# Optimization experiments

Measured on AMD Instinct MI355X. Metric: run time of the kernel, lower is better.

## Reference

```python
import jax, jax.numpy as jnp
import numpy as np

N = 100_000      # nodes
E = 1_600_000    # edges (avg degree 16)
C_IN = 128
HID = 128        # 2 * out_channels
OUT = 64
EDIM = 1
NEG_SLOPE = 0.2  # PyG GATConv default negative_slope


def _gat(x, src, dst, n, W, a_s, a_d, b, edge_attr=None, We=None, a_e=None):
    """PyG GATConv with heads=1, concat=True, add_self_loops=True (fill_value='mean').
    x: [n, Cin]; src/dst: [E] (messages flow src -> dst); returns [n, Cout].
    """
    xl = x @ W                 # [n, Cout] transformed node features
    a_src = xl @ a_s           # [n] per-node source attention logit
    a_dst = xl @ a_d           # [n] per-node destination attention logit
    loop = jnp.arange(n)
    if edge_attr is not None:
        # self-loop edge_attr = mean of incoming edge_attr per node (fill_value='mean')
        ones = jnp.ones((src.shape[0],), xl.dtype)
        cnt = jax.ops.segment_sum(ones, dst, num_segments=n)              # [n]
        s = jax.ops.segment_sum(edge_attr, dst, num_segments=n)           # [n, EDIM]
        loop_attr = jnp.where(cnt[:, None] > 0, s / jnp.maximum(cnt, 1.0)[:, None], 0.0)
        ea = jnp.concatenate([edge_attr, loop_attr], axis=0)              # [E+n, EDIM]
    src2 = jnp.concatenate([src, loop])
    dst2 = jnp.concatenate([dst, loop])
    alpha = a_src[src2] + a_dst[dst2]                                      # [E+n]
    if edge_attr is not None:
        alpha = alpha + (ea @ We) @ a_e                                    # edge-attribute attention term
    alpha = jax.nn.leaky_relu(alpha, NEG_SLOPE)
    # softmax over incoming edges of each destination node (stable)
    m = jax.ops.segment_max(alpha, dst2, num_segments=n)
    ex = jnp.exp(alpha - m[dst2])
    den = jax.ops.segment_sum(ex, dst2, num_segments=n)
    coef = ex / den[dst2]                                                  # [E+n]
    out = jax.ops.segment_sum(coef[:, None] * xl[src2], dst2, num_segments=n)
    return out + b


def setup_inputs() -> dict:
    key = jax.random.key(0)
    ks = jax.random.split(key, 32)
    s = 0.1
    inp = {
        "x": jax.random.normal(ks[0], (N, C_IN), jnp.float32),
        "edge_index": jax.random.randint(ks[1], (2, E), 0, N, jnp.int64),
        "edge_weights": jax.random.uniform(ks[2], (E, EDIM), jnp.float32),
    }
    def lin(k, i, o):
        return jax.random.normal(k, (i, o), jnp.float32) * s
    def vec(k, c):
        return jax.random.normal(k, (c,), jnp.float32) * s
    # layer 0: 128 -> 128 (with edge attention)
    inp["W0"], inp["as0"], inp["ad0"] = lin(ks[3], C_IN, HID), vec(ks[4], HID), vec(ks[5], HID)
    inp["ae0"], inp["We0"], inp["b0"] = vec(ks[6], HID), lin(ks[7], EDIM, HID), jnp.zeros((HID,), jnp.float32)
    # layer 1: 128 -> 128 (with edge attention)
    inp["W1"], inp["as1"], inp["ad1"] = lin(ks[8], HID, HID), vec(ks[9], HID), vec(ks[10], HID)
    inp["ae1"], inp["We1"], inp["b1"] = vec(ks[11], HID), lin(ks[12], EDIM, HID), jnp.zeros((HID,), jnp.float32)
    # conv_mu: 128 -> 64 (with edge attention)
    inp["Wm"], inp["asm"], inp["adm"] = lin(ks[13], HID, OUT), vec(ks[14], OUT), vec(ks[15], OUT)
    inp["aem"], inp["Wem"], inp["bm"] = vec(ks[16], OUT), lin(ks[17], EDIM, OUT), jnp.zeros((OUT,), jnp.float32)
    # conv_logstd: 128 -> 64 (called WITHOUT edge_attr -> no edge term)
    inp["Wl"], inp["asl"], inp["adl"] = lin(ks[18], HID, OUT), vec(ks[19], OUT), vec(ks[20], OUT)
    inp["bl"] = jnp.zeros((OUT,), jnp.float32)
    return inp


def reference(x, edge_index, edge_weights,
              W0, as0, ad0, ae0, We0, b0,
              W1, as1, ad1, ae1, We1, b1,
              Wm, asm, adm, aem, Wem, bm,
              Wl, asl, adl, bl):
    src, dst = edge_index[0], edge_index[1]
    h = jax.nn.relu(_gat(x, src, dst, N, W0, as0, ad0, b0, edge_weights, We0, ae0))
    h = jax.nn.relu(_gat(h, src, dst, N, W1, as1, ad1, b1, edge_weights, We1, ae1))
    mu = _gat(h, src, dst, N, Wm, asm, adm, bm, edge_weights, Wem, aem)
    logstd = _gat(h, src, dst, N, Wl, asl, adl, bl)  # no edge_attr, per original forward
    return mu, logstd
```

## Files before the change

### kernel.cpp

```cpp
#include <hip/hip_runtime.h>

#define NN 100000
#define EE 1600000

typedef __attribute__((ext_vector_type(8))) __bf16 bf16x8;
typedef __attribute__((ext_vector_type(4))) float f32x4;
typedef unsigned short u16;

__device__ __forceinline__ float bf2f(u16 v) {
  union { unsigned u; float f; } x; x.u = ((unsigned)v) << 16; return x.f;
}
__device__ __forceinline__ u16 f2bf(float f) {
  union { unsigned u; float f; } x; x.f = f;
  x.u += 0x7fffu + ((x.u >> 16) & 1u);
  return (u16)(x.u >> 16);
}
__device__ __forceinline__ float lo_f(unsigned u) {
  union { unsigned u; float f; } x; x.u = u << 16; return x.f;
}
__device__ __forceinline__ float hi_f(unsigned u) {
  union { unsigned u; float f; } x; x.u = u & 0xffff0000u; return x.f;
}
__device__ __forceinline__ float lrelu(float x) { return x > 0.f ? x : 0.2f * x; }
__device__ __forceinline__ int clampi(int v, int hi) {
  return ((unsigned)v < (unsigned)hi) ? v : 0;
}
__device__ __forceinline__ float ldf(const void* p, size_t i, int fl) {
  return fl ? ((const float*)p)[i] : bf2f(((const u16*)p)[i]);
}

__device__ __forceinline__ int wave_fdetect(const u16* __restrict__ xb) {
  int lane = threadIdx.x & 63;
  int bad = 0;
#pragma unroll
  for (int j = 0; j < 4; ++j) {
    float a = fabsf(bf2f(xb[lane * 4 + j]));
    bad |= (!(a == a) || a > 1e6f) ? 1 : 0;
  }
  return (__ballot(bad) != 0ull) ? 1 : 0;
}
__device__ __forceinline__ int wave_mdetect(const int* __restrict__ ei) {
  int lane = threadIdx.x & 63;
  int v = (lane < 32) ? ei[2 * lane + 1] : 0;
  return (__ballot(v != 0) == 0ull) ? 1 : 0;
}

__global__ void k_fillf(float* __restrict__ o, int n, float v) {
  int i = blockIdx.x * 256 + threadIdx.x;
  if (i < n) o[i] = v;
}

struct CvtDesc { const void* src; u16* dst; int n; };
struct SetupArgs {
  CvtDesc cvt[12];
  const void* W[4]; u16* WT[4]; int WM[4];
  const void* dw[3]; const void* da[3]; int dm[3];
  float* cvals;
  int* cnt;
  const u16* xb;
};
__global__ __launch_bounds__(256) void k_setup(SetupArgs a) {
  int b = blockIdx.x, t = threadIdx.x;
  const int ZB = (NN + 255) / 256;
  if (b < ZB) { int i = b * 256 + t; if (i < NN) a.cnt[i] = 0; return; }
  b -= ZB;
  if (b < 12) {
    int fl = wave_fdetect(a.xb);
    const void* src = a.cvt[b].src; u16* dst = a.cvt[b].dst; int n = a.cvt[b].n;
    for (int i = t; i < n; i += 256)
      dst[i] = fl ? f2bf(((const float*)src)[i]) : ((const u16*)src)[i];
    return;
  }
  b -= 12;
  if (b < 192) {
    int fl = wave_fdetect(a.xb);
    int wsel, lb;
    if (b < 64)       { wsel = 0; lb = b; }
    else if (b < 128) { wsel = 1; lb = b - 64; }
    else if (b < 160) { wsel = 2; lb = b - 128; }
    else              { wsel = 3; lb = b - 160; }
    int M = a.WM[wsel];
    int i = lb * 256 + t;
    if (i < 128 * M) {
      int k = i / M, m = i % M;
      a.WT[wsel][m * 128 + k] = f2bf(ldf(a.W[wsel], i, fl));
    }
    return;
  }
  b -= 192;
  if (b < 3) {
    if (t < 64) {
      int fl = wave_fdetect(a.xb);
      float s = 0.f; int m = a.dm[b];
      for (int j = t; j < m; j += 64) s += ldf(a.dw[b], j, fl) * ldf(a.da[b], j, fl);
      for (int off = 32; off; off >>= 1) s += __shfl_xor(s, off);
      if (t == 0) a.cvals[b] = s;
    }
    return;
  }
}

__global__ void k_bsum(const int* __restrict__ cnt, int* __restrict__ bsum, int n) {
  int b = blockIdx.x, t = threadIdx.x;
  int i0 = b * 1024 + t * 4;
  int s = 0;
#pragma unroll
  for (int j = 0; j < 4; ++j) { int i = i0 + j; if (i < n) s += cnt[i]; }
  for (int off = 32; off; off >>= 1) s += __shfl_xor(s, off);
  __shared__ int wt[4];
  int lane = t & 63, w = t >> 6;
  if (lane == 0) wt[w] = s;
  __syncthreads();
  if (t == 0) bsum[b] = wt[0] + wt[1] + wt[2] + wt[3];
}

__global__ void k_scanb(const int* __restrict__ bsum, int* __restrict__ boff, int nchunks) {
  int t = threadIdx.x;
  int lane = t & 63, w = t >> 6;
  int v = (t < nchunks) ? bsum[t] : 0;
  int sc = v;
  for (int off = 1; off < 64; off <<= 1) { int o = __shfl_up(sc, off); if (lane >= off) sc += o; }
  __shared__ int w0tot;
  if (w == 0 && lane == 63) w0tot = sc;
  __syncthreads();
  int incl = sc + (w ? w0tot : 0);
  if (t < nchunks) boff[t] = incl - v;
}

__global__ void k_scan_chunk(const int* __restrict__ cnt, const int* __restrict__ boff,
                             int* __restrict__ row_off, int n, int etot) {
  int b = blockIdx.x, t = threadIdx.x;
  int i0 = b * 1024 + t * 4;
  int v[4]; int s = 0;
#pragma unroll
  for (int j = 0; j < 4; ++j) { int i = i0 + j; v[j] = (i < n) ? cnt[i] : 0; s += v[j]; }
  int lane = t & 63, w = t >> 6;
  int sc = s;
  for (int off = 1; off < 64; off <<= 1) { int o = __shfl_up(sc, off); if (lane >= off) sc += o; }
  __shared__ int wt[4];
  if (lane == 63) wt[w] = sc;
  __syncthreads();
  int woff = 0;
  for (int k = 0; k < w; ++k) woff += wt[k];
  int ex = boff[b] + woff + sc - s;
#pragma unroll
  for (int j = 0; j < 4; ++j) { int i = i0 + j; if (i < n) row_off[i] = ex; ex += v[j]; }
  if (b == 0 && t == 0) row_off[n] = etot;
}

template<bool DUAL>
__device__ __forceinline__ void gemm_body(
    int bid, int fl, const void* __restrict__ Araw,
    const u16* __restrict__ WT,
    const u16* __restrict__ avs, const u16* __restrict__ avd,
    u16* __restrict__ xl,
    float* __restrict__ asrc, float* __restrict__ adst,
    float2* __restrict__ asAB, float* __restrict__ adstB, int n) {
  const int K = 128;
  int lane = threadIdx.x & 63;
  int wave = threadIdx.x >> 6;
  int quad = lane >> 4;
  int l16 = lane & 15;
  int r0 = (bid * 4 + wave) * 16;
  if (r0 >= n) return;
  int arow = r0 + l16; if (arow >= n) arow = n - 1;
  bf16x8 afr[4];
  if (fl) {
    const float* af = (const float*)Araw + (size_t)arow * K + quad * 8;
#pragma unroll
    for (int kb = 0; kb < 4; ++kb) {
      float4 f0 = *(const float4*)(af + kb * 32);
      float4 f1 = *(const float4*)(af + kb * 32 + 4);
      union { bf16x8 v; u16 s[8]; } t;
      t.s[0] = f2bf(f0.x); t.s[1] = f2bf(f0.y); t.s[2] = f2bf(f0.z); t.s[3] = f2bf(f0.w);
      t.s[4] = f2bf(f1.x); t.s[5] = f2bf(f1.y); t.s[6] = f2bf(f1.z); t.s[7] = f2bf(f1.w);
      afr[kb] = t.v;
    }
  } else {
    const u16* ab = (const u16*)Araw + (size_t)arow * K + quad * 8;
#pragma unroll
    for (int kb = 0; kb < 4; ++kb) afr[kb] = *(const bf16x8*)(ab + kb * 32);
  }
  f32x4 acc[8];
#pragma unroll
  for (int nb = 0; nb < 8; ++nb) acc[nb] = (f32x4){0.f, 0.f, 0.f, 0.f};
#pragma unroll
  for (int nb = 0; nb < 8; ++nb) {
    const u16* bbase = WT + (size_t)(nb * 16 + l16) * K + quad * 8;
#pragma unroll
    for (int kb = 0; kb < 4; ++kb) {
      bf16x8 bfr = *(const bf16x8*)(bbase + kb * 32);
      acc[nb] = __builtin_amdgcn_mfma_f32_16x16x32_bf16(afr[kb], bfr, acc[nb], 0, 0, 0);
    }
  }
  float ps[2][4] = {{0,0,0,0},{0,0,0,0}}, pd[2][4] = {{0,0,0,0},{0,0,0,0}};
#pragma unroll
  for (int nb = 0; nb < 8; ++nb) {
    const int g = (DUAL && nb >= 4) ? 1 : 0;
    int col = nb * 16 + l16;
    float vs = bf2f(avs[col]), vd = bf2f(avd[col]);
#pragma unroll
    for (int r = 0; r < 4; ++r) {
      int row = r0 + quad * 4 + r;
      float v = acc[nb][r];
      if (row < n) xl[(size_t)row * 128 + col] = f2bf(v);
      ps[g][r] += v * vs;
      pd[g][r] += v * vd;
    }
  }
#pragma unroll
  for (int off = 1; off < 16; off <<= 1) {
#pragma unroll
    for (int r = 0; r < 4; ++r) {
      ps[0][r] += __shfl_xor(ps[0][r], off);
      pd[0][r] += __shfl_xor(pd[0][r], off);
      if (DUAL) {
        ps[1][r] += __shfl_xor(ps[1][r], off);
        pd[1][r] += __shfl_xor(pd[1][r], off);
      }
    }
  }
  if (l16 == 0) {
#pragma unroll
    for (int r = 0; r < 4; ++r) {
      int row = r0 + quad * 4 + r;
      if (row < n) {
        if (DUAL) {
          asAB[row] = make_float2(ps[0][r], ps[1][r]);
          adst[row] = pd[0][r]; adstB[row] = pd[1][r];
        } else {
          asrc[row] = ps[0][r]; adst[row] = pd[0][r];
        }
      }
    }
  }
}

__global__ __launch_bounds__(256) void k_rkgemm(
    const int* __restrict__ ei, int* __restrict__ cnt, int* __restrict__ rank,
    const u16* __restrict__ xb, const void* __restrict__ Araw,
    const u16* __restrict__ WT, const u16* __restrict__ avs, const u16* __restrict__ avd,
    u16* __restrict__ xl, float* __restrict__ asrc, float* __restrict__ adst,
    int n, int gemmBlocks) {
  if ((int)blockIdx.x < gemmBlocks) {
    int fl = wave_fdetect(xb);
    gemm_body<false>(blockIdx.x, fl, Araw, WT, avs, avd, xl, asrc, adst,
                     nullptr, nullptr, n);
  } else {
    int m_ = wave_mdetect(ei);
    int e = ((int)blockIdx.x - gemmBlocks) * 256 + threadIdx.x;
    if (e >= EE) return;
    int d = m_ ? ei[2 * (size_t)(EE + e)] : ei[EE + e];
    d = clampi(d, NN);
    rank[e] = atomicAdd(&cnt[d], 1);
  }
}

template<bool DUAL>
__global__ __launch_bounds__(256) void k_gemm(
    const u16* __restrict__ A, const u16* __restrict__ WT,
    const u16* __restrict__ avs, const u16* __restrict__ avd,
    u16* __restrict__ xl, float* __restrict__ asrc, float* __restrict__ adst,
    float2* __restrict__ asAB, float* __restrict__ adstB, int n) {
  gemm_body<DUAL>(blockIdx.x, 0, A, WT, avs, avd, xl, asrc, adst, asAB, adstB, n);
}

__global__ void k_place(const int* __restrict__ ei, const void* __restrict__ ew,
                        const u16* __restrict__ xb,
                        const int* __restrict__ row_off, const int* __restrict__ rank,
                        int2* __restrict__ edges) {
  int m_ = wave_mdetect(ei);
  int fl = wave_fdetect(xb);
  int e = blockIdx.x * 256 + threadIdx.x;
  if (e >= EE) return;
  int s = m_ ? ei[2 * (size_t)e] : ei[e];
  int d = m_ ? ei[2 * (size_t)(EE + e)] : ei[EE + e];
  s = clampi(s, NN);
  d = clampi(d, NN);
  int p = row_off[d] + rank[e];
  if (p >= 0 && p < EE) edges[p] = make_int2(s, (int)f2bf(ldf(ew, e, fl)));
}

__global__ void k_loop2(const int* __restrict__ row_off, const int2* __restrict__ edges,
                        float* __restrict__ la, int n) {
  int i = blockIdx.x * 256 + threadIdx.x;
  if (i >= n) return;
  int b = row_off[i], e = row_off[i + 1];
  float s = 0.f;
  for (int j = b; j < e; ++j) s += bf2f((u16)(edges[j].y & 0xffff));
  la[i] = (e > b) ? s / (float)(e - b) : 0.f;
}

__global__ __launch_bounds__(256) void k_agg(
    const int* __restrict__ row_off, const int2* __restrict__ edges,
    const float* __restrict__ asrc, const float* __restrict__ adst,
    const float* __restrict__ la, const float* __restrict__ cptr,
    const u16* __restrict__ xl, const u16* __restrict__ bias,
    u16* __restrict__ out, int n) {
  __shared__ float lp[4][64];
  __shared__ int lsv[4][64];
  int wid = (blockIdx.x * blockDim.x + threadIdx.x) >> 6;
  if (wid >= n) return;
  int w = threadIdx.x >> 6;
  int d = __builtin_amdgcn_readfirstlane(wid);
  int lane = threadIdx.x & 63;
  float c = cptr[0];
  float ad = adst[d];
  float aL = lrelu(asrc[d] + ad + c * la[d]);
  float lsum = 0.f;
  unsigned su = *(const unsigned*)(xl + (size_t)d * 128 + 2 * lane);
  float A0 = lo_f(su), A1 = hi_f(su);
  int beg = row_off[d], end = row_off[d + 1];
  for (int base = beg; base < end; base += 64) {
    int i = base + lane;
    bool v = i < end;
    int2 ev = v ? edges[i] : make_int2(0, 0);
    int s = ev.x;
    float e = 0.f;
    if (v) {
      float al = lrelu(asrc[s] + ad + c * bf2f((u16)(ev.y & 0xffff)));
      e = __expf(al - aL);
    }
    lsum += e;
    lp[w][lane] = e; lsv[w][lane] = s;
    int cnt = end - base; if (cnt > 64) cnt = 64;
    float B0 = 0.f, B1 = 0.f, C0 = 0.f, C1 = 0.f, D0 = 0.f, D1 = 0.f;
    int j = 0;
    for (; j + 4 <= cnt; j += 4) {
      float p0 = lp[w][j + 0]; int s0 = lsv[w][j + 0];
      float p1 = lp[w][j + 1]; int s1 = lsv[w][j + 1];
      float p2 = lp[w][j + 2]; int s2 = lsv[w][j + 2];
      float p3 = lp[w][j + 3]; int s3 = lsv[w][j + 3];
      unsigned u0 = *(const unsigned*)(xl + (size_t)s0 * 128 + 2 * lane);
      unsigned u1 = *(const unsigned*)(xl + (size_t)s1 * 128 + 2 * lane);
      unsigned u2 = *(const unsigned*)(xl + (size_t)s2 * 128 + 2 * lane);
      unsigned u3 = *(const unsigned*)(xl + (size_t)s3 * 128 + 2 * lane);
      A0 = fmaf(p0, lo_f(u0), A0); A1 = fmaf(p0, hi_f(u0), A1);
      B0 = fmaf(p1, lo_f(u1), B0); B1 = fmaf(p1, hi_f(u1), B1);
      C0 = fmaf(p2, lo_f(u2), C0); C1 = fmaf(p2, hi_f(u2), C1);
      D0 = fmaf(p3, lo_f(u3), D0); D1 = fmaf(p3, hi_f(u3), D1);
    }
    for (; j < cnt; ++j) {
      float p0 = lp[w][j]; int s0 = lsv[w][j];
      unsigned u0 = *(const unsigned*)(xl + (size_t)s0 * 128 + 2 * lane);
      A0 = fmaf(p0, lo_f(u0), A0); A1 = fmaf(p0, hi_f(u0), A1);
    }
    A0 += B0 + C0 + D0; A1 += B1 + C1 + D1;
  }
#pragma unroll
  for (int off = 32; off; off >>= 1) lsum += __shfl_xor(lsum, off);
  float inv = 1.f / (lsum + 1.f);
  float o0 = fmaxf(fmaf(A0, inv, bf2f(bias[2 * lane])), 0.f);
  float o1 = fmaxf(fmaf(A1, inv, bf2f(bias[2 * lane + 1])), 0.f);
  unsigned uo = (unsigned)f2bf(o0) | ((unsigned)f2bf(o1) << 16);
  *(unsigned*)(out + (size_t)d * 128 + 2 * lane) = uo;
}

__global__ __launch_bounds__(256) void k_aggh(
    const int* __restrict__ row_off, const int2* __restrict__ edges,
    const float2* __restrict__ asAB, const float* __restrict__ adA,
    const float* __restrict__ adB,
    const float* __restrict__ la, const float* __restrict__ cptr,
    const u16* __restrict__ xl, const u16* __restrict__ bias,
    float* __restrict__ outf, int n) {
  __shared__ float lpA[4][64];
  __shared__ float lpB[4][64];
  __shared__ int lsv[4][64];
  int wid = (blockIdx.x * blockDim.x + threadIdx.x) >> 6;
  if (wid >= n) return;
  int w = threadIdx.x >> 6;
  int d = __builtin_amdgcn_readfirstlane(wid);
  int lane = threadIdx.x & 63;
  bool isMu = lane < 32;
  float c = cptr[0];
  float adAd = adA[d], adBd = adB[d];
  float2 abd = asAB[d];
  float aLA = lrelu(abd.x + adAd + c * la[d]);
  float aLB = lrelu(abd.y + adBd);
  float lsA = 0.f, lsB = 0.f;
  unsigned su = *(const unsigned*)(xl + (size_t)d * 128 + 2 * lane);
  float A0 = lo_f(su), A1 = hi_f(su);
  int beg = row_off[d], end = row_off[d + 1];
  for (int base = beg; base < end; base += 64) {
    int i = base + lane;
    bool v = i < end;
    int2 ev = v ? edges[i] : make_int2(0, 0);
    int s = ev.x;
    float eA = 0.f, eB = 0.f;
    if (v) {
      float2 ab = asAB[s];
      eA = __expf(lrelu(ab.x + adAd + c * bf2f((u16)(ev.y & 0xffff))) - aLA);
      eB = __expf(lrelu(ab.y + adBd) - aLB);
    }
    lsA += eA; lsB += eB;
    lpA[w][lane] = eA; lpB[w][lane] = eB; lsv[w][lane] = s;
    const float* lpp = isMu ? lpA[w] : lpB[w];
    int cnt = end - base; if (cnt > 64) cnt = 64;
    float B0 = 0.f, B1 = 0.f, C0 = 0.f, C1 = 0.f, D0 = 0.f, D1 = 0.f;
    int j = 0;
    for (; j + 4 <= cnt; j += 4) {
      float p0 = lpp[j + 0]; int s0 = lsv[w][j + 0];
      float p1 = lpp[j + 1]; int s1 = lsv[w][j + 1];
      float p2 = lpp[j + 2]; int s2 = lsv[w][j + 2];
      float p3 = lpp[j + 3]; int s3 = lsv[w][j + 3];
      unsigned u0 = *(const unsigned*)(xl + (size_t)s0 * 128 + 2 * lane);
      unsigned u1 = *(const unsigned*)(xl + (size_t)s1 * 128 + 2 * lane);
      unsigned u2 = *(const unsigned*)(xl + (size_t)s2 * 128 + 2 * lane);
      unsigned u3 = *(const unsigned*)(xl + (size_t)s3 * 128 + 2 * lane);
      A0 = fmaf(p0, lo_f(u0), A0); A1 = fmaf(p0, hi_f(u0), A1);
      B0 = fmaf(p1, lo_f(u1), B0); B1 = fmaf(p1, hi_f(u1), B1);
      C0 = fmaf(p2, lo_f(u2), C0); C1 = fmaf(p2, hi_f(u2), C1);
      D0 = fmaf(p3, lo_f(u3), D0); D1 = fmaf(p3, hi_f(u3), D1);
    }
    for (; j < cnt; ++j) {
      float p0 = lpp[j]; int s0 = lsv[w][j];
      unsigned u0 = *(const unsigned*)(xl + (size_t)s0 * 128 + 2 * lane);
      A0 = fmaf(p0, lo_f(u0), A0); A1 = fmaf(p0, hi_f(u0), A1);
    }
    A0 += B0 + C0 + D0; A1 += B1 + C1 + D1;
  }
#pragma unroll
  for (int off = 32; off; off >>= 1) {
    lsA += __shfl_xor(lsA, off);
    lsB += __shfl_xor(lsB, off);
  }
  float inv = 1.f / ((isMu ? lsA : lsB) + 1.f);
  int col0 = 2 * lane;
  float o0 = fmaf(A0, inv, bf2f(bias[col0]));
  float o1 = fmaf(A1, inv, bf2f(bias[col0 + 1]));
  float* ob = isMu ? (outf + (size_t)d * 64 + col0)
                   : (outf + (size_t)NN * 64 + (size_t)d * 64 + (col0 - 64));
  ob[0] = o0; ob[1] = o1;
}

extern "C" void kernel_launch(void* const* d_in, const int* in_sizes, int n_in,
                              void* d_out, int out_size, void* d_ws, size_t ws_size,
                              hipStream_t stream) {
  (void)in_sizes; (void)n_in;
  const int* ei = (const int*)d_in[1];
  const u16* xb = (const u16*)d_in[0];
  float* outf = (float*)d_out;

  u16* regionA = (u16*)d_out;
  u16* regionB = (u16*)d_out + (size_t)NN * 128;
  int* rank = (int*)d_out;

  char* p = (char*)d_ws;
  auto alloc = [&](size_t bytes) -> char* {
    char* r = p; p += (bytes + 255) & ~(size_t)255; return r;
  };
  int*   cnt    = (int*)alloc(NN * 4);
  int*   row_off= (int*)alloc((NN + 1) * 4);
  int*   bsum   = (int*)alloc(512);
  int*   boff   = (int*)alloc(512);
  float* la     = (float*)alloc(NN * 4);
  float* asrcA  = (float*)alloc(NN * 4);
  float* adstA  = (float*)alloc(NN * 4);
  float* adstB  = (float*)alloc(NN * 4);
  float2* asAB  = (float2*)alloc((size_t)NN * 8);
  int2*  edges  = (int2*)alloc((size_t)EE * 8);
  u16*   WT0    = (u16*)alloc(128 * 128 * 2);
  u16*   WT1    = (u16*)alloc(128 * 128 * 2);
  u16*   WTh    = (u16*)alloc(128 * 128 * 2);
  float* cvals  = (float*)alloc(16);
  u16*   vecc   = (u16*)alloc(9 * 256);
  u16*   xl     = (u16*)alloc((size_t)NN * 128 * 2);

  size_t NEED = (size_t)(p - (char*)d_ws);
  if (ws_size < NEED) {
    k_fillf<<<(out_size + 255) / 256, 256, 0, stream>>>(outf, out_size, 0.125f);
    return;
  }

  u16* as0c = vecc + 0 * 128; u16* ad0c = vecc + 1 * 128; u16* b0c = vecc + 2 * 128;
  u16* as1c = vecc + 3 * 128; u16* ad1c = vecc + 4 * 128; u16* b1c = vecc + 5 * 128;
  u16* hvs  = vecc + 6 * 128; u16* hvd  = vecc + 7 * 128; u16* bh  = vecc + 8 * 128;

  SetupArgs sa;
  sa.cvt[0]  = {d_in[4],  as0c, 128};
  sa.cvt[1]  = {d_in[5],  ad0c, 128};
  sa.cvt[2]  = {d_in[8],  b0c,  128};
  sa.cvt[3]  = {d_in[10], as1c, 128};
  sa.cvt[4]  = {d_in[11], ad1c, 128};
  sa.cvt[5]  = {d_in[14], b1c,  128};
  sa.cvt[6]  = {d_in[16], hvs,      64};
  sa.cvt[7]  = {d_in[22], hvs + 64, 64};
  sa.cvt[8]  = {d_in[17], hvd,      64};
  sa.cvt[9]  = {d_in[23], hvd + 64, 64};
  sa.cvt[10] = {d_in[20], bh,       64};
  sa.cvt[11] = {d_in[24], bh + 64,  64};
  sa.W[0] = d_in[3];  sa.WT[0] = WT0;            sa.WM[0] = 128;
  sa.W[1] = d_in[9];  sa.WT[1] = WT1;            sa.WM[1] = 128;
  sa.W[2] = d_in[15]; sa.WT[2] = WTh;            sa.WM[2] = 64;
  sa.W[3] = d_in[21]; sa.WT[3] = WTh + 64 * 128; sa.WM[3] = 64;
  sa.dw[0] = d_in[7];  sa.da[0] = d_in[6];  sa.dm[0] = 128;
  sa.dw[1] = d_in[13]; sa.da[1] = d_in[12]; sa.dm[1] = 128;
  sa.dw[2] = d_in[19]; sa.da[2] = d_in[18]; sa.dm[2] = 64;
  sa.cvals = cvals; sa.cnt = cnt; sa.xb = xb;
  const int ZB = (NN + 255) / 256;
  k_setup<<<ZB + 12 + 192 + 3, 256, 0, stream>>>(sa);

  const int Eblocks = (EE + 255) / 256;
  const int nchunks = (NN + 1023) / 1024;
  const int gblocks = (((NN + 15) / 16) + 3) / 4;
  const int eblocks = (int)(((size_t)NN * 64 + 255) / 256);

  k_rkgemm<<<gblocks + Eblocks, 256, 0, stream>>>(ei, cnt, rank, xb, d_in[0],
                                                  WT0, as0c, ad0c, xl, asrcA, adstA,
                                                  NN, gblocks);
  k_bsum<<<nchunks, 256, 0, stream>>>(cnt, bsum, NN);
  k_scanb<<<1, 128, 0, stream>>>(bsum, boff, nchunks);
  k_scan_chunk<<<nchunks, 256, 0, stream>>>(cnt, boff, row_off, NN, EE);
  k_place<<<Eblocks, 256, 0, stream>>>(ei, d_in[2], xb, row_off, rank, edges);
  k_loop2<<<(NN + 255) / 256, 256, 0, stream>>>(row_off, edges, la, NN);

  k_agg<<<eblocks, 256, 0, stream>>>(row_off, edges, asrcA, adstA, la,
                                     cvals + 0, xl, b0c, regionB, NN);
  k_gemm<false><<<gblocks, 256, 0, stream>>>(regionB, WT1, as1c, ad1c,
                                             xl, asrcA, adstA, nullptr, nullptr, NN);
  k_agg<<<eblocks, 256, 0, stream>>>(row_off, edges, asrcA, adstA, la,
                                     cvals + 1, xl, b1c, regionA, NN);
  k_gemm<true><<<gblocks, 256, 0, stream>>>(regionA, WTh, hvs, hvd,
                                            xl, nullptr, adstA, asAB, adstB, NN);
  k_aggh<<<eblocks, 256, 0, stream>>>(row_off, edges, asAB, adstA, adstB,
                                      la, cvals + 2, xl, bh, outf, NN);
}
```

Measured before the change: 565.4 us.

## Replace global-atomic CSR build with two-level bucketed radix sort of edges

Builds the destination-sorted CSR with a two-pass bucket sort instead of per-edge global atomics. Edges are first binned into 128-node buckets using per-block shared-memory histograms and a scan, then scattered to a staging buffer. Each bucket is then sorted locally in shared memory, which also yields row offsets and the mean self-loop edge weights. This removes the contended global atomicAdd pass, the separate rank array and the per-node loop2 pass. The cost is more kernels, staging through the xl buffer, and moving the layer-0 GEMM out of the fused launch so that it runs after the sort.

Result: faster. 536.8 us (-5.0%).

```diff
diff --git a/kernel.cpp b/kernel.cpp
--- a/kernel.cpp
+++ b/kernel.cpp
@@ -2,6 +2,10 @@
 
 #define NN 100000
 #define EE 1600000
+#define NBK 782
+#define NBKP 784
+#define NBLK 391
+#define NBLKP 392
 
 typedef __attribute__((ext_vector_type(8))) __bf16 bf16x8;
 typedef __attribute__((ext_vector_type(4))) float f32x4;
@@ -56,14 +60,10 @@
   const void* W[4]; u16* WT[4]; int WM[4];
   const void* dw[3]; const void* da[3]; int dm[3];
   float* cvals;
-  int* cnt;
   const u16* xb;
 };
 __global__ __launch_bounds__(256) void k_setup(SetupArgs a) {
   int b = blockIdx.x, t = threadIdx.x;
-  const int ZB = (NN + 255) / 256;
-  if (b < ZB) { int i = b * 256 + t; if (i < NN) a.cnt[i] = 0; return; }
-  b -= ZB;
   if (b < 12) {
     int fl = wave_fdetect(a.xb);
     const void* src = a.cvt[b].src; u16* dst = a.cvt[b].dst; int n = a.cvt[b].n;
@@ -100,52 +100,143 @@
   }
 }
 
-__global__ void k_bsum(const int* __restrict__ cnt, int* __restrict__ bsum, int n) {
+__global__ __launch_bounds__(256) void k_ehist(const int* __restrict__ ei,
+                                               int* __restrict__ histM) {
+  __shared__ int h[NBKP];
+  int blk = blockIdx.x, t = threadIdx.x;
+  int m_ = wave_mdetect(ei);
+  for (int j = t; j < NBKP; j += 256) h[j] = 0;
+  __syncthreads();
+#pragma unroll
+  for (int j = 0; j < 16; ++j) {
+    int e = blk * 4096 + j * 256 + t;
+    if (e < EE) {
+      int d = m_ ? ei[2 * (size_t)(EE + e)] : ei[EE + e];
+      d = clampi(d, NN);
+      atomicAdd(&h[d >> 7], 1);
+    }
+  }
+  __syncthreads();
+  for (int j = t; j < NBKP; j += 256) histM[j * NBLKP + blk] = h[j];
+}
+
+__global__ __launch_bounds__(512) void k_scanA(int* __restrict__ histM,
+                                               int* __restrict__ binTot) {
   int b = blockIdx.x, t = threadIdx.x;
-  int i0 = b * 1024 + t * 4;
-  int s = 0;
-#pragma unroll
-  for (int j = 0; j < 4; ++j) { int i = i0 + j; if (i < n) s += cnt[i]; }
-  for (int off = 32; off; off >>= 1) s += __shfl_xor(s, off);
-  __shared__ int wt[4];
+  int v = (t < NBLK) ? histM[b * NBLKP + t] : 0;
   int lane = t & 63, w = t >> 6;
-  if (lane == 0) wt[w] = s;
-  __syncthreads();
-  if (t == 0) bsum[b] = wt[0] + wt[1] + wt[2] + wt[3];
-}
-
-__global__ void k_scanb(const int* __restrict__ bsum, int* __restrict__ boff, int nchunks) {
+  int sc = v;
+  for (int off = 1; off < 64; off <<= 1) {
+    int o = __shfl_up(sc, off); if (lane >= off) sc += o;
+  }
+  __shared__ int wt[8];
+  if (lane == 63) wt[w] = sc;
+  __syncthreads();
+  int add = 0;
+  for (int k = 0; k < w; ++k) add += wt[k];
+  int excl = sc - v + add;
+  if (t < NBLK) histM[b * NBLKP + t] = excl;
+  if (t == 511) binTot[b] = excl;
+}
+
+__global__ __launch_bounds__(256) void k_scanB(const int* __restrict__ binTot,
+                                               int* __restrict__ bucketBase,
+                                               int* __restrict__ row_off) {
   int t = threadIdx.x;
-  int lane = t & 63, w = t >> 6;
-  int v = (t < nchunks) ? bsum[t] : 0;
-  int sc = v;
-  for (int off = 1; off < 64; off <<= 1) { int o = __shfl_up(sc, off); if (lane >= off) sc += o; }
-  __shared__ int w0tot;
-  if (w == 0 && lane == 63) w0tot = sc;
-  __syncthreads();
-  int incl = sc + (w ? w0tot : 0);
-  if (t < nchunks) boff[t] = incl - v;
-}
-
-__global__ void k_scan_chunk(const int* __restrict__ cnt, const int* __restrict__ boff,
-                             int* __restrict__ row_off, int n, int etot) {
-  int b = blockIdx.x, t = threadIdx.x;
-  int i0 = b * 1024 + t * 4;
   int v[4]; int s = 0;
 #pragma unroll
-  for (int j = 0; j < 4; ++j) { int i = i0 + j; v[j] = (i < n) ? cnt[i] : 0; s += v[j]; }
+  for (int j = 0; j < 4; ++j) {
+    int idx = t * 4 + j;
+    v[j] = (idx < NBK) ? binTot[idx] : 0;
+    s += v[j];
+  }
   int lane = t & 63, w = t >> 6;
   int sc = s;
-  for (int off = 1; off < 64; off <<= 1) { int o = __shfl_up(sc, off); if (lane >= off) sc += o; }
+  for (int off = 1; off < 64; off <<= 1) {
+    int o = __shfl_up(sc, off); if (lane >= off) sc += o;
+  }
   __shared__ int wt[4];
   if (lane == 63) wt[w] = sc;
   __syncthreads();
-  int woff = 0;
-  for (int k = 0; k < w; ++k) woff += wt[k];
-  int ex = boff[b] + woff + sc - s;
-#pragma unroll
-  for (int j = 0; j < 4; ++j) { int i = i0 + j; if (i < n) row_off[i] = ex; ex += v[j]; }
-  if (b == 0 && t == 0) row_off[n] = etot;
+  int add = 0;
+  for (int k = 0; k < w; ++k) add += wt[k];
+  int ex = add + sc - s;
+#pragma unroll
+  for (int j = 0; j < 4; ++j) {
+    int idx = t * 4 + j;
+    if (idx <= NBK) bucketBase[idx] = ex;
+    ex += v[j];
+  }
+  if (t == 0) row_off[NN] = EE;
+}
+
+__global__ __launch_bounds__(256) void k_escatter(
+    const int* __restrict__ ei, const void* __restrict__ ew,
+    const u16* __restrict__ xb, const int* __restrict__ histM,
+    const int* __restrict__ bucketBase, int2* __restrict__ stage) {
+  __shared__ int lbase[NBKP];
+  __shared__ int cur[NBKP];
+  int blk = blockIdx.x, t = threadIdx.x;
+  int m_ = wave_mdetect(ei);
+  int fl = wave_fdetect(xb);
+  for (int j = t; j < NBKP; j += 256) {
+    int bb = (j < NBK) ? (bucketBase[j] + histM[j * NBLKP + blk]) : 0;
+    lbase[j] = bb; cur[j] = 0;
+  }
+  __syncthreads();
+#pragma unroll
+  for (int j = 0; j < 16; ++j) {
+    int e = blk * 4096 + j * 256 + t;
+    if (e < EE) {
+      int s = m_ ? ei[2 * (size_t)e] : ei[e];
+      int d = m_ ? ei[2 * (size_t)(EE + e)] : ei[EE + e];
+      s = clampi(s, NN);
+      d = clampi(d, NN);
+      int bin = d >> 7, low = d & 127;
+      int r = atomicAdd(&cur[bin], 1);
+      int pos = lbase[bin] + r;
+      if (pos >= 0 && pos < EE)
+        stage[pos] = make_int2(s, (low << 16) | (int)f2bf(ldf(ew, e, fl)));
+    }
+  }
+}
+
+__global__ __launch_bounds__(256) void k_bucket(
+    const int2* __restrict__ stage, const int* __restrict__ bucketBase,
+    int2* __restrict__ edges, int* __restrict__ row_off, float* __restrict__ la) {
+  __shared__ int hist[128];
+  __shared__ float wsum[128];
+  __shared__ int pref[128];
+  __shared__ int cur[128];
+  int b = blockIdx.x, t = threadIdx.x;
+  int base = bucketBase[b], n = bucketBase[b + 1] - base;
+  if (t < 128) { hist[t] = 0; wsum[t] = 0.f; cur[t] = 0; }
+  __syncthreads();
+  for (int i = t; i < n; i += 256) {
+    int2 it = stage[base + i];
+    int bin = (it.y >> 16) & 127;
+    atomicAdd(&hist[bin], 1);
+    atomicAdd(&wsum[bin], bf2f((u16)(it.y & 0xffff)));
+  }
+  __syncthreads();
+  if (t == 0) {
+    int run = 0;
+    for (int j = 0; j < 128; ++j) { pref[j] = run; run += hist[j]; }
+  }
+  __syncthreads();
+  if (t < 128) {
+    int d = b * 128 + t;
+    if (d < NN) {
+      row_off[d] = base + pref[t];
+      la[d] = hist[t] ? wsum[t] / (float)hist[t] : 0.f;
+    }
+  }
+  for (int i = t; i < n; i += 256) {
+    int2 it = stage[base + i];
+    int bin = (it.y >> 16) & 127;
+    int r = atomicAdd(&cur[bin], 1);
+    edges[base + pref[bin] + r] = it;
+  }
 }
 
 template<bool DUAL>
@@ -236,24 +327,13 @@
   }
 }
 
-__global__ __launch_bounds__(256) void k_rkgemm(
-    const int* __restrict__ ei, int* __restrict__ cnt, int* __restrict__ rank,
+__global__ __launch_bounds__(256) void k_gemm0(
     const u16* __restrict__ xb, const void* __restrict__ Araw,
     const u16* __restrict__ WT, const u16* __restrict__ avs, const u16* __restrict__ avd,
-    u16* __restrict__ xl, float* __restrict__ asrc, float* __restrict__ adst,
-    int n, int gemmBlocks) {
-  if ((int)blockIdx.x < gemmBlocks) {
-    int fl = wave_fdetect(xb);
-    gemm_body<false>(blockIdx.x, fl, Araw, WT, avs, avd, xl, asrc, adst,
-                     nullptr, nullptr, n);
-  } else {
-    int m_ = wave_mdetect(ei);
-    int e = ((int)blockIdx.x - gemmBlocks) * 256 + threadIdx.x;
-    if (e >= EE) return;
-    int d = m_ ? ei[2 * (size_t)(EE + e)] : ei[EE + e];
-    d = clampi(d, NN);
-    rank[e] = atomicAdd(&cnt[d], 1);
-  }
+    u16* __restrict__ xl, float* __restrict__ asrc, float* __restrict__ adst, int n) {
+  int fl = wave_fdetect(xb);
+  gemm_body<false>(blockIdx.x, fl, Araw, WT, avs, avd, xl, asrc, adst,
+                   nullptr, nullptr, n);
 }
 
 template<bool DUAL>
@@ -263,32 +343,6 @@
     u16* __restrict__ xl, float* __restrict__ asrc, float* __restrict__ adst,
     float2* __restrict__ asAB, float* __restrict__ adstB, int n) {
   gemm_body<DUAL>(blockIdx.x, 0, A, WT, avs, avd, xl, asrc, adst, asAB, adstB, n);
-}
-
-__global__ void k_place(const int* __restrict__ ei, const void* __restrict__ ew,
-                        const u16* __restrict__ xb,
-                        const int* __restrict__ row_off, const int* __restrict__ rank,
-                        int2* __restrict__ edges) {
-  int m_ = wave_mdetect(ei);
-  int fl = wave_fdetect(xb);
-  int e = blockIdx.x * 256 + threadIdx.x;
-  if (e >= EE) return;
-  int s = m_ ? ei[2 * (size_t)e] : ei[e];
-  int d = m_ ? ei[2 * (size_t)(EE + e)] : ei[EE + e];
-  s = clampi(s, NN);
-  d = clampi(d, NN);
-  int p = row_off[d] + rank[e];
-  if (p >= 0 && p < EE) edges[p] = make_int2(s, (int)f2bf(ldf(ew, e, fl)));
-}
-
-__global__ void k_loop2(const int* __restrict__ row_off, const int2* __restrict__ edges,
-                        float* __restrict__ la, int n) {
-  int i = blockIdx.x * 256 + threadIdx.x;
-  if (i >= n) return;
-  int b = row_off[i], e = row_off[i + 1];
-  float s = 0.f;
-  for (int j = b; j < e; ++j) s += bf2f((u16)(edges[j].y & 0xffff));
-  la[i] = (e > b) ? s / (float)(e - b) : 0.f;
 }
 
 __global__ __launch_bounds__(256) void k_agg(
@@ -443,28 +497,29 @@
 
   u16* regionA = (u16*)d_out;
   u16* regionB = (u16*)d_out + (size_t)NN * 128;
-  int* rank = (int*)d_out;
+  int* histM = (int*)d_out;
 
   char* p = (char*)d_ws;
   auto alloc = [&](size_t bytes) -> char* {
     char* r = p; p += (bytes + 255) & ~(size_t)255; return r;
   };
-  int*   cnt    = (int*)alloc(NN * 4);
-  int*   row_off= (int*)alloc((NN + 1) * 4);
-  int*   bsum   = (int*)alloc(512);
-  int*   boff   = (int*)alloc(512);
-  float* la     = (float*)alloc(NN * 4);
-  float* asrcA  = (float*)alloc(NN * 4);
-  float* adstA  = (float*)alloc(NN * 4);
-  float* adstB  = (float*)alloc(NN * 4);
-  float2* asAB  = (float2*)alloc((size_t)NN * 8);
-  int2*  edges  = (int2*)alloc((size_t)EE * 8);
-  u16*   WT0    = (u16*)alloc(128 * 128 * 2);
-  u16*   WT1    = (u16*)alloc(128 * 128 * 2);
-  u16*   WTh    = (u16*)alloc(128 * 128 * 2);
-  float* cvals  = (float*)alloc(16);
-  u16*   vecc   = (u16*)alloc(9 * 256);
-  u16*   xl     = (u16*)alloc((size_t)NN * 128 * 2);
+  int*   row_off   = (int*)alloc((NN + 1) * 4);
+  int*   binTot    = (int*)alloc(NBKP * 4);
+  int*   bucketBase= (int*)alloc((NBKP + 2) * 4);
+  float* la        = (float*)alloc(NN * 4);
+  float* asrcA     = (float*)alloc(NN * 4);
+  float* adstA     = (float*)alloc(NN * 4);
+  float* adstB     = (float*)alloc(NN * 4);
+  float2* asAB     = (float2*)alloc((size_t)NN * 8);
+  int2*  edges     = (int2*)alloc((size_t)EE * 8);
+  u16*   WT0       = (u16*)alloc(128 * 128 * 2);
+  u16*   WT1       = (u16*)alloc(128 * 128 * 2);
+  u16*   WTh       = (u16*)alloc(128 * 128 * 2);
+  float* cvals     = (float*)alloc(16);
+  u16*   vecc      = (u16*)alloc(9 * 256);
+  u16*   xl        = (u16*)alloc((size_t)NN * 128 * 2);
+
+  int2* stage = (int2*)xl;
 
   size_t NEED = (size_t)(p - (char*)d_ws);
   if (ws_size < NEED) {
@@ -496,24 +551,20 @@
   sa.dw[0] = d_in[7];  sa.da[0] = d_in[6];  sa.dm[0] = 128;
   sa.dw[1] = d_in[13]; sa.da[1] = d_in[12]; sa.dm[1] = 128;
   sa.dw[2] = d_in[19]; sa.da[2] = d_in[18]; sa.dm[2] = 64;
-  sa.cvals = cvals; sa.cnt = cnt; sa.xb = xb;
-  const int ZB = (NN + 255) / 256;
-  k_setup<<<ZB + 12 + 192 + 3, 256, 0, stream>>>(sa);
-
-  const int Eblocks = (EE + 255) / 256;
-  const int nchunks = (NN + 1023) / 1024;
+  sa.cvals = cvals; sa.xb = xb;
+  k_setup<<<12 + 192 + 3, 256, 0, stream>>>(sa);
+
   const int gblocks = (((NN + 15) / 16) + 3) / 4;
   const int eblocks = (int)(((size_t)NN * 64 + 255) / 256);
 
-  k_rkgemm<<<gblocks + Eblocks, 256, 0, stream>>>(ei, cnt, rank, xb, d_in[0],
-                                                  WT0, as0c, ad0c, xl, asrcA, adstA,
-                                                  NN, gblocks);
-  k_bsum<<<nchunks, 256, 0, stream>>>(cnt, bsum, NN);
-  k_scanb<<<1, 128, 0, stream>>>(bsum, boff, nchunks);
-  k_scan_chunk<<<nchunks, 256, 0, stream>>>(cnt, boff, row_off, NN, EE);
-  k_place<<<Eblocks, 256, 0, stream>>>(ei, d_in[2], xb, row_off, rank, edges);
-  k_loop2<<<(NN + 255) / 256, 256, 0, stream>>>(row_off, edges, la, NN);
-
+  k_ehist<<<NBLK, 256, 0, stream>>>(ei, histM);
+  k_scanA<<<NBK, 512, 0, stream>>>(histM, binTot);
+  k_scanB<<<1, 256, 0, stream>>>(binTot, bucketBase, row_off);
+  k_escatter<<<NBLK, 256, 0, stream>>>(ei, d_in[2], xb, histM, bucketBase, stage);
+  k_bucket<<<NBK, 256, 0, stream>>>(stage, bucketBase, edges, row_off, la);
+
+  k_gemm0<<<gblocks, 256, 0, stream>>>(xb, d_in[0], WT0, as0c, ad0c,
+                                       xl, asrcA, adstA, NN);
   k_agg<<<eblocks, 256, 0, stream>>>(row_off, edges, asrcA, adstA, la,
                                      cvals + 0, xl, b0c, regionB, NN);
   k_gemm<false><<<gblocks, 256, 0, stream>>>(regionB, WT1, as1c, ad1c,
```
